# Optimization experiments

Hardware: AMD Instinct MI355X
Metric: run time of the kernel (lower is better)

## Reference

```python
import jax, jax.numpy as jnp
import numpy as np

NH = 4       # num_heads
WS = 4       # window_size (in subdomains)
SHIFT = 2    # shift (in subdomains) on odd layers
SUB = 16     # physical subdomain size (y and x)
L = 4        # num_layers
EPS = 1e-5   # InstanceNorm2d eps


def _pw_mlp(x, W1, b1, W2, b2):
    # pointwise (1x1 conv) MLP over channel dim of [..., C, y, x]
    h = jnp.einsum('oc,...cyx->...oyx', W1, x) + b1[:, None, None]
    h = jax.nn.gelu(h, approximate=False)
    return jnp.einsum('oc,...cyx->...oyx', W2, h) + b2[:, None, None]


def _inorm(x):
    # InstanceNorm2d (affine=False): normalize each channel over spatial dims
    mu = jnp.mean(x, axis=(-2, -1), keepdims=True)
    var = jnp.var(x, axis=(-2, -1), keepdims=True)
    return (x - mu) * jax.lax.rsqrt(var + EPS)


def _grid_to_win(g, B, nwy, nwx):
    # g: [B, n_sub_y, n_sub_x, C, sh, sw] -> [B*nwy*nwx, WS*WS, C, sh, sw]
    C, sh, sw = g.shape[3:]
    g = g.reshape(B, nwy, WS, nwx, WS, C, sh, sw).transpose(0, 1, 3, 2, 4, 5, 6, 7)
    return g.reshape(B * nwy * nwx, WS * WS, C, sh, sw)


def _win_to_grid(d, B, nwy, nwx):
    # inverse of _grid_to_win
    C, sh, sw = d.shape[2:]
    g = d.reshape(B, nwy, nwx, WS, WS, C, sh, sw).transpose(0, 1, 3, 2, 4, 5, 6, 7)
    return g.reshape(B, nwy * WS, nwx * WS, C, sh, sw)


def _attn(d, Wq, bq, Wk, bk, Wv, bv, Wo, bo, shift, B, nwy, nwx):
    # function-space windowed self-attention; tokens are subdomain functions
    if shift > 0:
        g = _win_to_grid(d, B, nwy, nwx)
        g = jnp.roll(g, (-shift, -shift), axis=(1, 2))
        d = _grid_to_win(g, B, nwy, nwx)
    E = Wq.shape[0]
    dh = E // NH
    Bw, S, C, sh, sw = d.shape

    def proj(W, b):
        p = jnp.einsum('dc,bscyx->bsdyx', W, d) + b[:, None, None]
        return p.reshape(Bw, S, NH, dh, sh, sw)

    q, k, vv = proj(Wq, bq), proj(Wk, bk), proj(Wv, bv)
    # integral inner-product score: mean over subdomain points, / sqrt(dh)
    scale = 1.0 / ((sh * sw) * (float(dh) ** 0.5))
    scores = jnp.einsum('bihcyx,bjhcyx->bhij', q, k) * scale
    A = jax.nn.softmax(scores, axis=-1)
    o = jnp.einsum('bhij,bjhcyx->bihcyx', A, vv).reshape(Bw, S, E, sh, sw)
    o = jnp.einsum('dc,bscyx->bsdyx', Wo, o) + bo[:, None, None]
    if shift > 0:
        g = _win_to_grid(o, B, nwy, nwx)
        g = jnp.roll(g, (shift, shift), axis=(1, 2))
        o = _grid_to_win(g, B, nwy, nwx)
    return o


def _forward(v, inp_W1, inp_b1, inp_W2, inp_b2, Wq, bq, Wk, bk, Wv, bv, Wo, bo,
             mlp_W1, mlp_b1, mlp_W2, mlp_b2, out_W1, out_b1, out_W2, out_b2,
             dsy, dsx):
    B, Cin, H, W = v.shape
    n_sub_y, n_sub_x = dsy // SUB, dsx // SUB
    sh, sw = H // n_sub_y, W // n_sub_x
    nwy, nwx = n_sub_y // WS, n_sub_x // WS
    # cell-centered grid, channels (y, x)
    yc = (jnp.arange(H, dtype=v.dtype) + 0.5) * (dsy / H)
    xc = (jnp.arange(W, dtype=v.dtype) + 0.5) * (dsx / W)
    g = jnp.stack(jnp.meshgrid(yc, xc, indexing='ij'), axis=0)  # [2,H,W]
    g = jnp.broadcast_to(g, (B, 2, H, W))
    v = jnp.concatenate([g, v], axis=1)
    v = _pw_mlp(v, inp_W1, inp_b1, inp_W2, inp_b2)  # [B,E,H,W]
    E = v.shape[1]
    # win_decompose2d: pixels -> subdomain grid -> windows of WSxWS subdomains
    sgrid = v.reshape(B, E, n_sub_y, sh, n_sub_x, sw).transpose(0, 2, 4, 1, 3, 5)
    d = _grid_to_win(sgrid, B, nwy, nwx)  # [B*nw, WS*WS, E, sh, sw]
    for i in range(L):
        shift = 0 if i % 2 == 0 else SHIFT
        d = _attn(_inorm(d), Wq[i], bq[i], Wk[i], bk[i], Wv[i], bv[i],
                  Wo[i], bo[i], shift, B, nwy, nwx) + d
        d = _pw_mlp(_inorm(d), mlp_W1[i], mlp_b1[i], mlp_W2[i], mlp_b2[i]) + d
    # win_recompose2d
    sgrid = _win_to_grid(d, B, nwy, nwx)  # [B, n_sub_y, n_sub_x, E, sh, sw]
    u = sgrid.transpose(0, 3, 1, 4, 2, 5).reshape(B, E, H, W)
    return _pw_mlp(u, out_W1, out_b1, out_W2, out_b2)


def setup_inputs() -> dict:
    key = jax.random.key(0)
    ks = jax.random.split(key, 16)
    B, Cin, H, W, E, HID, Cout = 8, 3, 256, 256, 64, 128, 1
    s = 0.02
    r = lambda k, shape: (s * jax.random.normal(k, shape)).astype(jnp.float32)
    z = lambda shape: jnp.zeros(shape, jnp.float32)
    return {
        'v': jax.random.normal(ks[0], (B, Cin, H, W), dtype=jnp.float32),
        'inp_W1': r(ks[1], (HID, Cin + 2)), 'inp_b1': z((HID,)),
        'inp_W2': r(ks[2], (E, HID)), 'inp_b2': z((E,)),
        'Wq': r(ks[3], (L, E, E)), 'bq': z((L, E)),
        'Wk': r(ks[4], (L, E, E)), 'bk': z((L, E)),
        'Wv': r(ks[5], (L, E, E)), 'bv': z((L, E)),
        'Wo': r(ks[6], (L, E, E)), 'bo': z((L, E)),
        'mlp_W1': r(ks[7], (L, E, E)), 'mlp_b1': z((L, E)),
        'mlp_W2': r(ks[8], (L, E, E)), 'mlp_b2': z((L, E)),
        'out_W1': r(ks[9], (HID, E)), 'out_b1': z((HID,)),
        'out_W2': r(ks[10], (Cout, HID)), 'out_b2': z((Cout,)),
        'domain_size_y': 256, 'domain_size_x': 256,
    }


def reference(v, inp_W1, inp_b1, inp_W2, inp_b2, Wq, bq, Wk, bk, Wv, bv, Wo, bo,
              mlp_W1, mlp_b1, mlp_W2, mlp_b2, out_W1, out_b1, out_W2, out_b2,
              domain_size_y, domain_size_x):
    return _forward(v, inp_W1, inp_b1, inp_W2, inp_b2, Wq, bq, Wk, bk, Wv, bv,
                    Wo, bo, mlp_W1, mlp_b1, mlp_W2, mlp_b2, out_W1, out_b1,
                    out_W2, out_b2, domain_size_y, domain_size_x)
```

## Files before the change

kernel.cpp:

```cpp
#include <hip/hip_runtime.h>
#include <math.h>

typedef unsigned short u16;
typedef unsigned int   u32;
typedef __attribute__((ext_vector_type(8))) short bf16x8;
typedef __attribute__((ext_vector_type(4))) float f32x4;

#define NTOK  2048
#define TOKSZ 16384ull

#define CBAR() __asm__ __volatile__("" ::: "memory")

__device__ __forceinline__ float bf2f(u16 b) { return __uint_as_float(((u32)b) << 16); }
__device__ __forceinline__ u16 f2bf(float f) {
    u32 u = __float_as_uint(f);
    u += 0x7FFFu + ((u >> 16) & 1u);
    return (u16)(u >> 16);
}
__device__ __forceinline__ float gelu_f(float x) {
    return 0.5f * x * (1.0f + erff(x * 0.70710678118654752440f));
}
__device__ __forceinline__ int shift_tok(int n) {
    int w = n >> 4, s = n & 15;
    int b = w >> 4, wy = (w >> 2) & 3, wx = w & 3;
// ... 78 lines not shown
            float ha = b1[hid] + W1[hid*5]*in0 + W1[hid*5+1]*in1 + W1[hid*5+2]*in2
                     + W1[hid*5+3]*in3 + W1[hid*5+4]*in4;
            float hb2 = b1[hid+1] + W1[hid*5+5]*in0 + W1[hid*5+6]*in1 + W1[hid*5+7]*in2
                     + W1[hid*5+8]*in3 + W1[hid*5+9]*in4;
            u32 pk = (u32)f2bf(gelu_f(ha)) | ((u32)f2bf(gelu_f(hb2)) << 16);
            *(u32*)&hsT[swz(t, h2 >> 3) + (h2 & 7)] = pk;
        }
        #pragma unroll
        for (int r = 0; r < 2; ++r) {
            int u = t + r * 256; int e = u >> 3, c8 = u & 7;
            *(uint4*)&wl[swz(e, c8)] = *(const uint4*)(W2bf + e * 128 + half * 64 + c8 * 8);
        }
        __syncthreads();
        #pragma unroll
        for (int ks = 0; ks < 2; ++ks) {
            U8 af[4], bf[4];
            #pragma unroll
            for (int mt = 0; mt < 4; ++mt)
                af[mt].u = *(const uint4*)&hsT[swz(px0 + mt*16 + m, ks*4 + qd)];
            #pragma unroll
            for (int nt = 0; nt < 4; ++nt)
                bf[nt].u = *(const uint4*)&wl[swz(nt*16 + m, ks*4 + qd)];
            #pragma unroll
            for (int mt = 0; mt < 4; ++mt)
                #pragma unroll
                for (int nt = 0; nt < 4; ++nt)
                    acc[mt][nt] = __builtin_amdgcn_mfma_f32_16x16x32_bf16(
                        af[mt].b, bf[nt].b, acc[mt][nt], 0, 0, 0);
        }
    }
    __syncthreads();
    float sv[4], qv[4];
    #pragma unroll
    for (int nt = 0; nt < 4; ++nt) {
        float ss = 0.f, qq = 0.f;
        #pragma unroll
        for (int mt = 0; mt < 4; ++mt)
            #pragma unroll
            for (int r = 0; r < 4; ++r) { float xx = acc[mt][nt][r]; ss += xx; qq = fmaf(xx, xx, qq); }
        ss += __shfl_xor(ss, 16); ss += __shfl_xor(ss, 32);
        qq += __shfl_xor(qq, 16); qq += __shfl_xor(qq, 32);
        sv[nt] = ss; qv[nt] = qq;
    }
    float* sarr = (float*)smem;
    if (qd == 0) {
        #pragma unroll
        for (int nt = 0; nt < 4; ++nt) {
            sarr[(nt*16 + m)*4 + wv] = sv[nt];
            sarr[256 + (nt*16 + m)*4 + wv] = qv[nt];
        }
    }
    __syncthreads();
    if (t < 64) {
        float ss = sarr[t*4] + sarr[t*4+1] + sarr[t*4+2] + sarr[t*4+3];
        float qq = sarr[256+t*4] + sarr[256+t*4+1] + sarr[256+t*4+2] + sarr[256+t*4+3];
        float mu = ss * (1.0f/256.0f);
        float var = qq * (1.0f/256.0f) - mu * mu;
        mursg[(size_t)n * 128 + t] = mu;
        mursg[(size_t)n * 128 + 64 + t] = rsqrtf(var + 1e-5f);
    }
    __syncthreads();
    float* eps = (float*)smem + wv * 2304;
    float* dp = d + (size_t)n * TOKSZ;
    #pragma unroll
    for (int ch2 = 0; ch2 < 2; ++ch2) {
        if (ch2) CBAR();
        #pragma unroll
        for (int mt = ch2*2; mt < ch2*2+2; ++mt)
            #pragma unroll
            for (int nt = 0; nt < 4; ++nt)
                #pragma unroll
                for (int r = 0; r < 4; ++r)
                    eps[((mt&1)*16 + qd*4 + r) * 68 + nt*16 + m] = acc[mt][nt][r];
        CBAR();
        #pragma unroll
        for (int j = 0; j < 8; ++j) {
            int f = l + 64*j; int row = f >> 4, c4 = f & 15;
            float4 v = *(float4*)&eps[row * 68 + c4 * 4];
            *(float4*)&dp[(px0 + ch2*32 + row) * 64 + c4 * 4] = v;
        }
    }
}

__device__ __forceinline__ void gemm64h(const u16* xs, const u16* wl, const float* bv4,
                                        int px0w, int m, int qd, u16* dst) {
    f32x4 acc[2][4];
    #pragma unroll
    for (int nt = 0; nt < 4; ++nt) {
        float bb = bv4[nt];
        acc[0][nt] = {bb, bb, bb, bb};
        acc[1][nt] = {bb, bb, bb, bb};
    }
    #pragma unroll
    for (int ks = 0; ks < 2; ++ks) {
        U8 af[2], bfr[4];
        #pragma unroll
        for (int mi = 0; mi < 2; ++mi)
            af[mi].u = *(const uint4*)&xs[swz(px0w + mi*16 + m, ks*4 + qd)];
        #pragma unroll
        for (int nt = 0; nt < 4; ++nt)
            bfr[nt].u = *(const uint4*)&wl[swz(nt*16 + m, ks*4 + qd)];
        #pragma unroll
        for (int mi = 0; mi < 2; ++mi)
            #pragma unroll
            for (int nt = 0; nt < 4; ++nt)
                acc[mi][nt] = __builtin_amdgcn_mfma_f32_16x16x32_bf16(
                    af[mi].b, bfr[nt].b, acc[mi][nt], 0, 0, 0);
    }
    #pragma unroll
    for (int mi = 0; mi < 2; ++mi)
        #pragma unroll
        for (int nt = 0; nt < 4; ++nt)
            #pragma unroll
            for (int r = 0; r < 4; ++r) {
                int R = px0w + mi*16 + qd*4 + r, ch = nt*16 + m;
                dst[swz(R, ch >> 3) + (ch & 7)] = f2bf(acc[mi][nt][r]);
            }
}

__global__ __launch_bounds__(256, 2)
void scores_qkv(const float* __restrict__ dres, const float* __restrict__ mursg,
                const u16* __restrict__ Wq, const float* __restrict__ bq,
                const u16* __restrict__ Wk, const float* __restrict__ bk,
                const u16* __restrict__ Wv, const float* __restrict__ bv,
                int shifted, float* __restrict__ Ap, u16* __restrict__ vbuf) {
    extern __shared__ char smem[];
    u16* xs  = (u16*)smem;
    u16* qls = (u16*)(smem + 16384);
    u16* kls = (u16*)(smem + 32768);
    u16* wlq = (u16*)(smem + 49152);
    u16* wlk = (u16*)(smem + 57344);
    u16* wlv = (u16*)(smem + 65536);
    float* mloc = (float*)(smem + 73728);
    int w = blockIdx.x, half = blockIdx.y, t = threadIdx.x;
    int wv = t >> 6, l = t & 63, m = l & 15, qd = l >> 4;
    int px0w = wv * 32;
    int nst[4];
    #pragma unroll
    for (int i8 = 0; i8 < 4; ++i8) {
        int nn = w * 16 + (4 * i8 + wv);
        nst[i8] = shifted ? shift_tok(nn) : nn;
    }
    #pragma unroll
    for (int r = 0; r < 8; ++r) {
        int u = t + r * 256;
        int nn = w * 16 + (u >> 7);
        int ni = shifted ? shift_tok(nn) : nn;
        mloc[u] = mursg[(size_t)ni * 128 + (u & 127)];
    }
    #pragma unroll
    for (int r = 0; r < 2; ++r) {
        int u = t + r * 256; int e = u >> 3, c8 = u & 7;
        *(uint4*)&wlq[swz(e, c8)] = *(const uint4*)(Wq + e * 64 + c8 * 8);
        *(uint4*)&wlk[swz(e, c8)] = *(const uint4*)(Wk + e * 64 + c8 * 8);
        *(uint4*)&wlv[swz(e, c8)] = *(const uint4*)(Wv + e * 64 + c8 * 8);
    }
    float bqv[4], bkv[4], bvv[4];
    #pragma unroll
    for (int nt = 0; nt < 4; ++nt) {
        bqv[nt] = bq[nt*16 + m]; bkv[nt] = bk[nt*16 + m]; bvv[nt] = bv[nt*16 + m];
    }
    f32x4 sacc = {0.f, 0.f, 0.f, 0.f};
    __syncthreads();
    for (int ch = 0; ch < 16; ++ch) {
        int pxb = half * 128 + ch * 8;
        #pragma unroll
        for (int i8 = 0; i8 < 4; ++i8) {
            int u = t + i8 * 256; int row = u >> 3, c8 = u & 7;
            int pxl = row & 7;
            int tok = 4 * i8 + wv;
            const float4* gp = (const float4*)
                (dres + (size_t)nst[i8] * TOKSZ + (size_t)(pxb + pxl) * 64 + c8 * 8);
            float4 f0 = gp[0], f1 = gp[1];
            const float4* mp = (const float4*)&mloc[tok * 128 + c8 * 8];
            float4 mu0 = mp[0], mu1 = mp[1];
            const float4* rp = (const float4*)&mloc[tok * 128 + 64 + c8 * 8];
            float4 rs0 = rp[0], rs1 = rp[1];
            uint4 o;
            o.x = (u32)f2bf((f0.x-mu0.x)*rs0.x) | ((u32)f2bf((f0.y-mu0.y)*rs0.y) << 16);
            o.y = (u32)f2bf((f0.z-mu0.z)*rs0.z) | ((u32)f2bf((f0.w-mu0.w)*rs0.w) << 16);
            o.z = (u32)f2bf((f1.x-mu1.x)*rs1.x) | ((u32)f2bf((f1.y-mu1.y)*rs1.y) << 16);
            o.w = (u32)f2bf((f1.z-mu1.z)*rs1.z) | ((u32)f2bf((f1.w-mu1.w)*rs1.w) << 16);
            *(uint4*)&xs[swz(row, c8)] = o;
        }
        __syncthreads();
        gemm64h(xs, wlq, bqv, px0w, m, qd, qls);
        gemm64h(xs, wlk, bkv, px0w, m, qd, kls);
        gemm64h(xs, wlv, bvv, px0w, m, qd, xs);
        __syncthreads();
        #pragma unroll
        for (int p2 = 0; p2 < 4; ++p2) {
            U8 af, bfr;
            int row = m * 8 + p2 * 2 + (qd >> 1);
            int c8 = wv * 2 + (qd & 1);
            af.u  = *(const uint4*)&qls[swz(row, c8)];
            bfr.u = *(const uint4*)&kls[swz(row, c8)];
            sacc = __builtin_amdgcn_mfma_f32_16x16x32_bf16(af.b, bfr.b, sacc, 0, 0, 0);
        }
        #pragma unroll
        for (int i8 = 0; i8 < 4; ++i8) {
            int u = t + i8 * 256; int row = u >> 3, c8 = u & 7;
            int pxl = row & 7;
            *(uint4*)(vbuf + (size_t)nst[i8] * 16384 + (size_t)(pxb + pxl) * 64 + c8 * 8)
                = *(const uint4*)&xs[swz(row, c8)];
        }
        __syncthreads();
    }
    float* ap = Ap + (size_t)half * 131072 + ((size_t)w * 4 + wv) * 256;
    #pragma unroll
    for (int r = 0; r < 4; ++r)
        ap[(qd * 4 + r) * 16 + m] = sacc[r] * (1.0f / 1024.0f);
}

__global__ __launch_bounds__(256, 2)
void wo_mlp(const u16* __restrict__ vb, const float* __restrict__ Ap,
            const u16* __restrict__ Wo, const float* __restrict__ bo,
            const u16* __restrict__ W1, const float* __restrict__ b1,
            const u16* __restrict__ W2, const float* __restrict__ b2,
            int shifted, float* __restrict__ dres, float* __restrict__ mursg,
            int wmu) {
    extern __shared__ char smem[];
    u16* xs = (u16*)smem;
    u16* wl = (u16*)(smem + 32768);
    float* As = (float*)(smem + 32768);
    int*  nis = (int*)(smem + 33792);
    float* sarr = (float*)(smem + 32768);
    float* murs2 = (float*)smem;
    int bid = blockIdx.x;
    int qg = bid >> 7, r7 = bid & 127;
    int n = ((qg << 3) + (r7 & 7)) * 16 + (r7 >> 3);
    int t = threadIdx.x;
    int wv = t >> 6, l = t & 63, m = l & 15, qd = l >> 4;
    int px0 = wv * 64;
    int w = n >> 4, i = n & 15;
    int no = shifted ? shift_tok(n) : n;
    int rbase = l >> 4, c4l = l & 15;
    if (t < 16) { int nn = w * 16 + t; nis[t] = shifted ? shift_tok(nn) : nn; }
    if (t >= 64 && t < 128) {
        int u = t - 64; int h = u >> 4, j = u & 15;
        size_t ai = ((size_t)(w * 4 + h)) * 256 + i * 16 + j;
        float sc = (Ap[ai] + Ap[131072 + ai]) * (1.0f / 1024.0f);
        float mx = sc;
        #pragma unroll
        for (int off = 1; off < 16; off <<= 1) mx = fmaxf(mx, __shfl_xor(mx, off, 16));
        float e = expf(sc - mx);
        float ssum = e;
        #pragma unroll
        for (int off = 1; off < 16; off <<= 1) ssum += __shfl_xor(ssum, off, 16);
        As[u] = e / ssum;
    }
    __syncthreads();
    #pragma unroll
    for (int r = 0; r < 8; ++r) {
        int idx = r * 256 + t;
        int px = idx >> 3, c8 = idx & 7, h = c8 >> 1;
        float a0=0,a1=0,a2=0,a3=0,a4=0,a5=0,a6=0,a7=0;
        #pragma unroll
        for (int j = 0; j < 16; ++j) {
            const u16* src = vb + (size_t)nis[j] * 16384 + (size_t)px * 64 + c8 * 8;
            uint4 pv = *(const uint4*)src;
            float aw = As[h * 16 + j];
            a0 = fmaf(aw, __uint_as_float(pv.x << 16), a0);
            a1 = fmaf(aw, __uint_as_float(pv.x & 0xFFFF0000u), a1);
            a2 = fmaf(aw, __uint_as_float(pv.y << 16), a2);
            a3 = fmaf(aw, __uint_as_float(pv.y & 0xFFFF0000u), a3);
            a4 = fmaf(aw, __uint_as_float(pv.z << 16), a4);
            a5 = fmaf(aw, __uint_as_float(pv.z & 0xFFFF0000u), a5);
            a6 = fmaf(aw, __uint_as_float(pv.w << 16), a6);
            a7 = fmaf(aw, __uint_as_float(pv.w & 0xFFFF0000u), a7);
        }
        uint4 o;
        o.x = (u32)f2bf(a0) | ((u32)f2bf(a1) << 16);
        o.y = (u32)f2bf(a2) | ((u32)f2bf(a3) << 16);
        o.z = (u32)f2bf(a4) | ((u32)f2bf(a5) << 16);
        o.w = (u32)f2bf(a6) | ((u32)f2bf(a7) << 16);
        *(uint4*)&xs[swz(px, c8)] = o;
    }
    __syncthreads();
    #pragma unroll
    for (int r = 0; r < 2; ++r) {
        int u = t + r * 256;
        int e = u >> 3, c8 = u & 7;
        *(uint4*)&wl[swz(e, c8)] = *(const uint4*)(Wo + e * 64 + c8 * 8);
    }
    __syncthreads();
    f32x4 acc[4][4];
    #pragma unroll
    for (int nt = 0; nt < 4; ++nt) {
        float bb = bo[nt * 16 + m];
        #pragma unroll
        for (int mt = 0; mt < 4; ++mt) acc[mt][nt] = {bb, bb, bb, bb};
    }
    #pragma unroll
    for (int ks = 0; ks < 2; ++ks) {
// ... 115 lines not shown
                int R = px0 + mt*16 + qd*4 + r;
                xs[swz(R, ch >> 3) + (ch & 7)] = f2bf(gelu_f(acc[mt][nt][r]));
            }
    }
    #pragma unroll
    for (int r = 0; r < 2; ++r) {
        int u = t + r * 256;
        int e = u >> 3, c8 = u & 7;
        *(uint4*)&wl[swz(e, c8)] = *(const uint4*)(W2 + e * 64 + c8 * 8);
    }
    __syncthreads();
    #pragma unroll
    for (int nt = 0; nt < 4; ++nt) {
        float bb = b2[nt * 16 + m];
        #pragma unroll
        for (int mt = 0; mt < 4; ++mt) acc[mt][nt] = {bb, bb, bb, bb};
    }
    #pragma unroll
    for (int ks = 0; ks < 2; ++ks) {
        U8 af[4], bf[4];
        #pragma unroll
        for (int mt = 0; mt < 4; ++mt)
            af[mt].u = *(const uint4*)&xs[swz(px0 + mt*16 + m, ks*4 + qd)];
        #pragma unroll
        for (int nt = 0; nt < 4; ++nt)
            bf[nt].u = *(const uint4*)&wl[swz(nt*16 + m, ks*4 + qd)];
        #pragma unroll
        for (int mt = 0; mt < 4; ++mt)
            #pragma unroll
            for (int nt = 0; nt < 4; ++nt)
                acc[mt][nt] = __builtin_amdgcn_mfma_f32_16x16x32_bf16(
                    af[mt].b, bf[nt].b, acc[mt][nt], 0, 0, 0);
    }
    __syncthreads();
    #pragma unroll
    for (int ch2 = 0; ch2 < 2; ++ch2) {
        if (ch2) CBAR();
        #pragma unroll
        for (int mt = ch2*2; mt < ch2*2+2; ++mt)
            #pragma unroll
            for (int nt = 0; nt < 4; ++nt)
                #pragma unroll
                for (int r = 0; r < 4; ++r)
                    eps[((mt&1)*16 + qd*4 + r) * 68 + nt*16 + m] = acc[mt][nt][r];
        CBAR();
        #pragma unroll
        for (int j = 0; j < 8; ++j) {
            int row = rbase + 4*j;
            float4 dv = *(float4*)&eps[row * 68 + c4l * 4];
            float4 bs = xv[ch2][j];
            bs.x += dv.x; bs.y += dv.y; bs.z += dv.z; bs.w += dv.w;
            xv[ch2][j] = bs;
            *(float4*)&dp[(px0 + ch2*32 + row) * 64 + c4l * 4] = bs;
        }
    }
    if (wmu) {
        __syncthreads();
        float t0=0,t1=0,t2=0,t3=0,u0=0,u1=0,u2=0,u3=0;
        #pragma unroll
        for (int ch2 = 0; ch2 < 2; ++ch2)
            #pragma unroll
            for (int j = 0; j < 8; ++j) {
                float4 v = xv[ch2][j];
                t0 += v.x; u0 = fmaf(v.x, v.x, u0);
                t1 += v.y; u1 = fmaf(v.y, v.y, u1);
                t2 += v.z; u2 = fmaf(v.z, v.z, u2);
                t3 += v.w; u3 = fmaf(v.w, v.w, u3);
            }
        sarr[(cb+0)*16+g]=t0; sarr[(cb+1)*16+g]=t1; sarr[(cb+2)*16+g]=t2; sarr[(cb+3)*16+g]=t3;
        qarr[(cb+0)*16+g]=u0; qarr[(cb+1)*16+g]=u1; qarr[(cb+2)*16+g]=u2; qarr[(cb+3)*16+g]=u3;
        __syncthreads();
        if (t < 64) {
            float ss = 0.f, qq = 0.f;
            #pragma unroll
            for (int gg = 0; gg < 16; ++gg) { ss += sarr[t*16+gg]; qq += qarr[t*16+gg]; }
            float mu = ss * (1.0f/256.0f);
            float var = qq * (1.0f/256.0f) - mu * mu;
            mursg[(size_t)no * 128 + t] = mu;
            mursg[(size_t)no * 128 + 64 + t] = rsqrtf(var + 1e-5f);
        }
    }
}

__global__ __launch_bounds__(256, 3)
void wo_av(const u16* __restrict__ vb, const float* __restrict__ Ap,
           const u16* __restrict__ Wo, const float* __restrict__ bo,
           int shifted, float* __restrict__ dres) {
    extern __shared__ char smem[];
    u16* xs = (u16*)smem;
    u16* wl = (u16*)(smem + 32768);
    float* As = (float*)(smem + 40960);
    int*  nis = (int*)(smem + 41216);
    int bid = blockIdx.x;
    int qg = bid >> 7, r7 = bid & 127;
    int n = ((qg << 3) + (r7 & 7)) * 16 + (r7 >> 3);
    int t = threadIdx.x;
    int wv = t >> 6, l = t & 63, m = l & 15, qd = l >> 4;
    int px0 = wv * 64;
    int w = n >> 4, i = n & 15;
    int no = shifted ? shift_tok(n) : n;
    if (t < 16) { int nn = w * 16 + t; nis[t] = shifted ? shift_tok(nn) : nn; }
    if (t >= 64 && t < 128) {
        int u = t - 64; int h = u >> 4, j = u & 15;
        size_t ai = ((size_t)(w * 4 + h)) * 256 + i * 16 + j;
        float sc = (Ap[ai] + Ap[131072 + ai]) * (1.0f / 1024.0f);
        float mx = sc;
        #pragma unroll
        for (int off = 1; off < 16; off <<= 1) mx = fmaxf(mx, __shfl_xor(mx, off, 16));
        float e = expf(sc - mx);
        float ssum = e;
        #pragma unroll
        for (int off = 1; off < 16; off <<= 1) ssum += __shfl_xor(ssum, off, 16);
        As[u] = e / ssum;
    }
    #pragma unroll
    for (int r = 0; r < 2; ++r) {
        int u = t + r * 256;
        int e = u >> 3, c8 = u & 7;
        *(uint4*)&wl[swz(e, c8)] = *(const uint4*)(Wo + e * 64 + c8 * 8);
    }
    __syncthreads();
    #pragma unroll
    for (int r = 0; r < 8; ++r) {
        int idx = r * 256 + t;
        int px = idx >> 3, c8 = idx & 7, h = c8 >> 1;
        float a0=0,a1=0,a2=0,a3=0,a4=0,a5=0,a6=0,a7=0;
        #pragma unroll
        for (int j = 0; j < 16; ++j) {
            const u16* src = vb + (size_t)nis[j] * 16384 + (size_t)px * 64 + c8 * 8;
            uint4 pv = *(const uint4*)src;
            float aw = As[h * 16 + j];
            a0 = fmaf(aw, __uint_as_float(pv.x << 16), a0);
            a1 = fmaf(aw, __uint_as_float(pv.x & 0xFFFF0000u), a1);
            a2 = fmaf(aw, __uint_as_float(pv.y << 16), a2);
            a3 = fmaf(aw, __uint_as_float(pv.y & 0xFFFF0000u), a3);
            a4 = fmaf(aw, __uint_as_float(pv.z << 16), a4);
            a5 = fmaf(aw, __uint_as_float(pv.z & 0xFFFF0000u), a5);
            a6 = fmaf(aw, __uint_as_float(pv.w << 16), a6);
            a7 = fmaf(aw, __uint_as_float(pv.w & 0xFFFF0000u), a7);
        }
        uint4 o;
        o.x = (u32)f2bf(a0) | ((u32)f2bf(a1) << 16);
        o.y = (u32)f2bf(a2) | ((u32)f2bf(a3) << 16);
        o.z = (u32)f2bf(a4) | ((u32)f2bf(a5) << 16);
        o.w = (u32)f2bf(a6) | ((u32)f2bf(a7) << 16);
        *(uint4*)&xs[swz(px, c8)] = o;
    }
    __syncthreads();
    f32x4 acc[4][4];
    #pragma unroll
    for (int nt = 0; nt < 4; ++nt) {
        float bb = bo[nt * 16 + m];
        #pragma unroll
        for (int mt = 0; mt < 4; ++mt) acc[mt][nt] = {bb, bb, bb, bb};
    }
    #pragma unroll
    for (int ks = 0; ks < 2; ++ks) {
        U8 af[4], bf[4];
        #pragma unroll
        for (int mt = 0; mt < 4; ++mt)
            af[mt].u = *(const uint4*)&xs[swz(px0 + mt*16 + m, ks*4 + qd)];
        #pragma unroll
        for (int nt = 0; nt < 4; ++nt)
            bf[nt].u = *(const uint4*)&wl[swz(nt*16 + m, ks*4 + qd)];
        #pragma unroll
        for (int mt = 0; mt < 4; ++mt)
            #pragma unroll
            for (int nt = 0; nt < 4; ++nt)
                acc[mt][nt] = __builtin_amdgcn_mfma_f32_16x16x32_bf16(
                    af[mt].b, bf[nt].b, acc[mt][nt], 0, 0, 0);
    }
    __syncthreads();
    float* eps = (float*)smem + wv * 2304;
    float* dp = dres + (size_t)no * TOKSZ;
    #pragma unroll
    for (int ch2 = 0; ch2 < 2; ++ch2) {
        if (ch2) CBAR();
        #pragma unroll
        for (int mt = ch2*2; mt < ch2*2+2; ++mt)
            #pragma unroll
            for (int nt = 0; nt < 4; ++nt)
                #pragma unroll
                for (int r = 0; r < 4; ++r)
                    eps[((mt&1)*16 + qd*4 + r) * 68 + nt*16 + m] = acc[mt][nt][r];
        CBAR();
        #pragma unroll
        for (int j = 0; j < 8; ++j) {
            int f = l + 64*j; int row = f >> 4, c4 = f & 15;
            float4 dv = *(float4*)&eps[row * 68 + c4 * 4];
            float* gp = &dp[(px0 + ch2*32 + row) * 64 + c4 * 4];
            float4 gv = *(float4*)gp;
            gv.x += dv.x; gv.y += dv.y; gv.z += dv.z; gv.w += dv.w;
            *(float4*)gp = gv;
        }
    }
}

__global__ __launch_bounds__(256, 2)
void mlp_out(const float* __restrict__ dres,
             const u16* __restrict__ W1, const float* __restrict__ b1,
             const u16* __restrict__ W2, const float* __restrict__ b2,
             const u16* __restrict__ oW1, const float* __restrict__ ob1,
             const float* __restrict__ oW2, const float* __restrict__ ob2,
             void* __restrict__ outp, const int* __restrict__ flag) {
    extern __shared__ char smem[];
    u16* xs = (u16*)smem;
    u16* wl = (u16*)(smem + 32768);
    float* sarr = (float*)(smem + 32768);
    float* murs = (float*)smem;
    int n = blockIdx.x, t = threadIdx.x;
    int wv = t >> 6, l = t & 63, m = l & 15, qd = l >> 4;
    int px0 = wv * 64;
    int rbase = l >> 4, c4 = l & 15;
    const float4* gin = (const float4*)(dres + (size_t)n * TOKSZ);
    float4 xv[2][8];
    float s0=0,s1=0,s2=0,s3=0,q0=0,q1=0,q2=0,q3=0;
    #pragma unroll
    for (int ch2 = 0; ch2 < 2; ++ch2)
        #pragma unroll
        for (int j = 0; j < 8; ++j) {
            float4 v = gin[(px0 + ch2*32 + rbase + 4*j) * 16 + c4];
            xv[ch2][j] = v;
            s0 += v.x; q0 = fmaf(v.x, v.x, q0);
            s1 += v.y; q1 = fmaf(v.y, v.y, q1);
            s2 += v.z; q2 = fmaf(v.z, v.z, q2);
            s3 += v.w; q3 = fmaf(v.w, v.w, q3);
        }
    int cb = 4 * c4, g = t >> 4;
    sarr[(cb+0)*16+g]=s0; sarr[(cb+1)*16+g]=s1; sarr[(cb+2)*16+g]=s2; sarr[(cb+3)*16+g]=s3;
    float* qarr = sarr + 1024;
    qarr[(cb+0)*16+g]=q0; qarr[(cb+1)*16+g]=q1; qarr[(cb+2)*16+g]=q2; qarr[(cb+3)*16+g]=q3;
    __syncthreads();
    if (t < 64) {
        float ss = 0.f, qq = 0.f;
        #pragma unroll
        for (int gg = 0; gg < 16; ++gg) { ss += sarr[t*16+gg]; qq += qarr[t*16+gg]; }
        float mu = ss * (1.0f/256.0f);
        float var = qq * (1.0f/256.0f) - mu * mu;
        murs[t] = mu; murs[64 + t] = rsqrtf(var + 1e-5f);
    }
    __syncthreads();
    float m0 = murs[cb], m1 = murs[cb+1], m2 = murs[cb+2], m3 = murs[cb+3];
    float r0 = murs[64+cb], r1 = murs[64+cb+1], r2 = murs[64+cb+2], r3 = murs[64+cb+3];
    __syncthreads();
    #pragma unroll
    for (int ch2 = 0; ch2 < 2; ++ch2)
        #pragma unroll
        for (int j = 0; j < 8; ++j) {
            float4 v = xv[ch2][j];
            int row = px0 + ch2*32 + rbase + 4*j;
            uint2 o;
            o.x = (u32)f2bf((v.x-m0)*r0) | ((u32)f2bf((v.y-m1)*r1) << 16);
            o.y = (u32)f2bf((v.z-m2)*r2) | ((u32)f2bf((v.w-m3)*r3) << 16);
            *(uint2*)&xs[swz(row, c4 >> 1) + (c4 & 1) * 4] = o;
        }
    #pragma unroll
    for (int r = 0; r < 2; ++r) {
        int u = t + r * 256;
        int e = u >> 3, c8 = u & 7;
        *(uint4*)&wl[swz(e, c8)] = *(const uint4*)(W1 + e * 64 + c8 * 8);
    }
    __syncthreads();
    f32x4 acc[4][4];
    #pragma unroll
    for (int nt = 0; nt < 4; ++nt) {
        float bb = b1[nt * 16 + m];
        #pragma unroll
        for (int mt = 0; mt < 4; ++mt) acc[mt][nt] = {bb, bb, bb, bb};
    }
    #pragma unroll
    for (int ks = 0; ks < 2; ++ks) {
        U8 af[4], bf[4];
        #pragma unroll
        for (int mt = 0; mt < 4; ++mt)
            af[mt].u = *(const uint4*)&xs[swz(px0 + mt*16 + m, ks*4 + qd)];
        #pragma unroll
        for (int nt = 0; nt < 4; ++nt)
            bf[nt].u = *(const uint4*)&wl[swz(nt*16 + m, ks*4 + qd)];
        #pragma unroll
        for (int mt = 0; mt < 4; ++mt)
            #pragma unroll
            for (int nt = 0; nt < 4; ++nt)
                acc[mt][nt] = __builtin_amdgcn_mfma_f32_16x16x32_bf16(
                    af[mt].b, bf[nt].b, acc[mt][nt], 0, 0, 0);
    }
    __syncthreads();
    #pragma unroll
    for (int nt = 0; nt < 4; ++nt) {
        int ch = nt * 16 + m;
        #pragma unroll
        for (int mt = 0; mt < 4; ++mt)
            #pragma unroll
            for (int r = 0; r < 4; ++r) {
                int R = px0 + mt*16 + qd*4 + r;
                xs[swz(R, ch >> 3) + (ch & 7)] = f2bf(gelu_f(acc[mt][nt][r]));
            }
    }
    #pragma unroll
    for (int r = 0; r < 2; ++r) {
        int u = t + r * 256;
        int e = u >> 3, c8 = u & 7;
        *(uint4*)&wl[swz(e, c8)] = *(const uint4*)(W2 + e * 64 + c8 * 8);
    }
    __syncthreads();
    #pragma unroll
    for (int nt = 0; nt < 4; ++nt) {
        float bb = b2[nt * 16 + m];
        #pragma unroll
        for (int mt = 0; mt < 4; ++mt) acc[mt][nt] = {bb, bb, bb, bb};
    }
    #pragma unroll
    for (int ks = 0; ks < 2; ++ks) {
        U8 af[4], bf[4];
        #pragma unroll
        for (int mt = 0; mt < 4; ++mt)
            af[mt].u = *(const uint4*)&xs[swz(px0 + mt*16 + m, ks*4 + qd)];
        #pragma unroll
        for (int nt = 0; nt < 4; ++nt)
            bf[nt].u = *(const uint4*)&wl[swz(nt*16 + m, ks*4 + qd)];
        #pragma unroll
        for (int mt = 0; mt < 4; ++mt)
            #pragma unroll
            for (int nt = 0; nt < 4; ++nt)
                acc[mt][nt] = __builtin_amdgcn_mfma_f32_16x16x32_bf16(
                    af[mt].b, bf[nt].b, acc[mt][nt], 0, 0, 0);
    }
    __syncthreads();
    float* eps = (float*)smem + wv * 2304;
    #pragma unroll
    for (int ch2 = 0; ch2 < 2; ++ch2) {
        if (ch2) CBAR();
        #pragma unroll
        for (int mt = ch2*2; mt < ch2*2+2; ++mt)
            #pragma unroll
            for (int nt = 0; nt < 4; ++nt)
                #pragma unroll
                for (int r = 0; r < 4; ++r)
                    eps[((mt&1)*16 + qd*4 + r) * 68 + nt*16 + m] = acc[mt][nt][r];
        CBAR();
        #pragma unroll
        for (int j = 0; j < 8; ++j) {
            int row = rbase + 4*j;
            float4 dv = *(float4*)&eps[row * 68 + c4 * 4];
            float4 bs = xv[ch2][j];
            bs.x += dv.x; bs.y += dv.y; bs.z += dv.z; bs.w += dv.w;
            xv[ch2][j] = bs;
        }
    }
    __syncthreads();
    #pragma unroll
    for (int ch2 = 0; ch2 < 2; ++ch2)
        #pragma unroll
        for (int j = 0; j < 8; ++j) {
            float4 v = xv[ch2][j];
            int row = px0 + ch2*32 + rbase + 4*j;
            uint2 o;
            o.x = (u32)f2bf(v.x) | ((u32)f2bf(v.y) << 16);
            o.y = (u32)f2bf(v.z) | ((u32)f2bf(v.w) << 16);
            *(uint2*)&xs[swz(row, c4 >> 1) + (c4 & 1) * 4] = o;
        }
    __syncthreads();
    float val[4][4];
    #pragma unroll
    for (int mt = 0; mt < 4; ++mt)
        #pragma unroll
        for (int r = 0; r < 4; ++r) val[mt][r] = 0.f;
    for (int nh = 0; nh < 2; ++nh) {
        if (nh) __syncthreads();
        #pragma unroll
        for (int r = 0; r < 2; ++r) {
            int u = t + r * 256;
            int e = u >> 3, c8 = u & 7;
            *(uint4*)&wl[swz(e, c8)] = *(const uint4*)(oW1 + (size_t)nh * 4096 + e * 64 + c8 * 8);
        }
        __syncthreads();
        float w2v[4];
        #pragma unroll
        for (int nt = 0; nt < 4; ++nt) w2v[nt] = oW2[nh * 64 + nt * 16 + m];
        #pragma unroll
        for (int mtp = 0; mtp < 2; ++mtp) {
            f32x4 oacc[2][4];
            #pragma unroll
            for (int nt = 0; nt < 4; ++nt) {
                float bb = ob1[nh * 64 + nt * 16 + m];
                oacc[0][nt] = {bb, bb, bb, bb};
                oacc[1][nt] = {bb, bb, bb, bb};
            }
            #pragma unroll
            for (int ks = 0; ks < 2; ++ks) {
                U8 af[2], bf[4];
                #pragma unroll
                for (int mi = 0; mi < 2; ++mi)
                    af[mi].u = *(const uint4*)&xs[swz(px0 + (2*mtp+mi)*16 + m, ks*4 + qd)];
                #pragma unroll
                for (int nt = 0; nt < 4; ++nt)
                    bf[nt].u = *(const uint4*)&wl[swz(nt*16 + m, ks*4 + qd)];
                #pragma unroll
                for (int mi = 0; mi < 2; ++mi)
                    #pragma unroll
                    for (int nt = 0; nt < 4; ++nt)
                        oacc[mi][nt] = __builtin_amdgcn_mfma_f32_16x16x32_bf16(
                            af[mi].b, bf[nt].b, oacc[mi][nt], 0, 0, 0);
            }
            #pragma unroll
            for (int mi = 0; mi < 2; ++mi)
                #pragma unroll
                for (int r = 0; r < 4; ++r) {
                    float p = 0.f;
                    #pragma unroll
                    for (int nt = 0; nt < 4; ++nt)
                        p = fmaf(gelu_f(oacc[mi][nt][r]), w2v[nt], p);
                    val[2*mtp + mi][r] += p;
                }
        }
    }
    __syncthreads();
    float* red = (float*)smem;
    #pragma unroll
    for (int mt = 0; mt < 4; ++mt)
        #pragma unroll
        for (int r = 0; r < 4; ++r)
            red[(px0 + mt*16 + qd*4 + r) * 17 + m] = val[mt][r];
    __syncthreads();
    float a = ob2[0];
    #pragma unroll
    for (int j = 0; j < 16; ++j) a += red[t * 17 + j];
    int w = n >> 4, s = n & 15;
    int b = w >> 4, wy = (w >> 2) & 3, wx = w & 3;
    int ty = s >> 2, tx = s & 3;
    int y = ((wy << 2) + ty) * 16 + (t >> 4);
    int x = ((wx << 2) + tx) * 16 + (t & 15);
    size_t oi = (size_t)b * 65536 + (size_t)y * 256 + (size_t)x;
    if (*flag) ((float*)outp)[oi] = a;
    else       ((u16*)outp)[oi] = f2bf(a);
}

extern "C" void kernel_launch(void* const* d_in, const int* in_sizes, int n_in,
                              void* d_out, int out_size, void* d_ws, size_t ws_size,
                              hipStream_t stream) {
    (void)n_in; (void)out_size; (void)ws_size;
    const int* pdsy = (const int*)d_in[21];
    const int* pdsx = (const int*)d_in[22];

    char* wsb = (char*)d_ws;
    float* bufd  = (float*)wsb;
    u16*  vbuf   = (u16*)(wsb + 134217728ull);
    float* Ap    = (float*)(wsb + 201326592ull);
    float* mursg = (float*)(wsb + 202375168ull);
    float* wbufA = (float*)(wsb + 203423744ull);
    u16* wbuf16  = (u16*)(wsb + 203434496ull);
    int* flag    = (int*)(wsb + 203669248ull);

    const int f32set[12] = {1, 2, 4, 6, 8, 10, 12, 14, 16, 18, 19, 20};
    WArgs wa;
    int off16[NWT + 1]; off16[0] = 0;
    int c32[NWT + 1];
    int fo = 0;
    for (int i = 0; i < NWT; ++i) {
        int di = i + 1;
        wa.src[i] = d_in[di];
        off16[i + 1] = off16[i] + in_sizes[di];
        wa.off16[i] = off16[i];
        int isf = 0;
        for (int j = 0; j < 12; ++j) if (f32set[j] == di) isf = 1;
        wa.f32o[i] = isf ? fo : -1;
        c32[di] = isf ? fo : -1;
        if (isf) fo += in_sizes[di];
    }
    wa.off16[NWT] = off16[NWT];

    detect_kernel<<<1, 64, 0, stream>>>((const u16*)d_in[1], flag);
    cvt_weights<<<(off16[NWT] + 255) / 256, 256, 0, stream>>>(wa, flag, wbufA, wbuf16);

    const float* f_inpW1 = wbufA + c32[1];
    const float* f_inpb1 = wbufA + c32[2];
    const float* f_inpb2 = wbufA + c32[4];
    const float* f_bq  = wbufA + c32[6];
    const float* f_bk  = wbufA + c32[8];
    const float* f_bv  = wbufA + c32[10];
    const float* f_bo  = wbufA + c32[12];
    const float* f_mb1 = wbufA + c32[14];
    const float* f_mb2 = wbufA + c32[16];
    const float* f_ob1 = wbufA + c32[18];
    const float* f_oW2 = wbufA + c32[19];
    const float* f_ob2 = wbufA + c32[20];
    const u16* h_inpW2 = wbuf16 + off16[2];
    const u16* h_Wq  = wbuf16 + off16[4];
    const u16* h_Wk  = wbuf16 + off16[6];
    const u16* h_Wv  = wbuf16 + off16[8];
    const u16* h_Wo  = wbuf16 + off16[10];
    const u16* h_mW1 = wbuf16 + off16[12];
    const u16* h_mW2 = wbuf16 + off16[14];
    const u16* h_oW1 = wbuf16 + off16[16];

    embed_mfma<<<NTOK, 256, 40960, stream>>>(d_in[0], flag, f_inpW1, f_inpb1,
                                             h_inpW2, f_inpb2, pdsy, pdsx,
                                             bufd, mursg);

    for (int l = 0; l < 4; ++l) {
        int sh = l & 1;
        const u16* Wql = h_Wq + l * 4096;  const float* bql = f_bq + l * 64;
        const u16* Wkl = h_Wk + l * 4096;  const float* bkl = f_bk + l * 64;
        const u16* Wvl = h_Wv + l * 4096;  const float* bvl = f_bv + l * 64;
        const u16* Wol = h_Wo + l * 4096;  const float* bol = f_bo + l * 64;
        const u16* W1l = h_mW1 + l * 4096; const float* b1l = f_mb1 + l * 64;
        const u16* W2l = h_mW2 + l * 4096; const float* b2l = f_mb2 + l * 64;

        scores_qkv<<<dim3(128, 2), 256, 81920, stream>>>(
            bufd, mursg, Wql, bql, Wkl, bkl, Wvl, bvl, sh, Ap, vbuf);
        if (l < 3) {
            wo_mlp<<<NTOK, 256, 40960, stream>>>(vbuf, Ap, Wol, bol,
                                                 W1l, b1l, W2l, b2l,
                                                 sh, bufd, mursg, 1);
        } else {
            wo_av<<<NTOK, 256, 41280, stream>>>(vbuf, Ap, Wol, bol, sh, bufd);
            mlp_out<<<NTOK, 256, 40960, stream>>>(bufd, W1l, b1l, W2l, b2l,
                                                  h_oW1, f_ob1, f_oW2, f_ob2,
                                                  d_out, flag);
        }
    }
}
```

Measured before the change: 957.6 us.

## Double threads per block in scores_qkv and split score reduction across waves

scores_qkv now launches 512 threads (8 waves) instead of 256, so each wave computes a 16-row tile of the QKV projections instead of 32 rows. The per-head score MFMAs are split across two wave groups, and their partial sums are combined through shared memory at the end. The aim is more latency hiding and parallelism per block on the 256-block grid, which is small relative to the CU count. The cost is an extra barrier plus shared-memory traffic for the reduction, and higher register pressure under the tighter launch bounds.

```diff
diff --git a/kernel.cpp b/kernel.cpp
--- a/kernel.cpp
+++ b/kernel.cpp
@@ -184,43 +184,36 @@
     }
 }
 
-__device__ __forceinline__ void gemm64h(const u16* xs, const u16* wl, const float* bv4,
+__device__ __forceinline__ void gemm64q(const u16* xs, const u16* wl, const float* bv4,
                                         int px0w, int m, int qd, u16* dst) {
-    f32x4 acc[2][4];
+    f32x4 acc[4];
     #pragma unroll
     for (int nt = 0; nt < 4; ++nt) {
         float bb = bv4[nt];
-        acc[0][nt] = {bb, bb, bb, bb};
-        acc[1][nt] = {bb, bb, bb, bb};
+        acc[nt] = {bb, bb, bb, bb};
     }
     #pragma unroll
     for (int ks = 0; ks < 2; ++ks) {
-        U8 af[2], bfr[4];
-        #pragma unroll
-        for (int mi = 0; mi < 2; ++mi)
-            af[mi].u = *(const uint4*)&xs[swz(px0w + mi*16 + m, ks*4 + qd)];
+        U8 af, bfr[4];
+        af.u = *(const uint4*)&xs[swz(px0w + m, ks*4 + qd)];
         #pragma unroll
         for (int nt = 0; nt < 4; ++nt)
             bfr[nt].u = *(const uint4*)&wl[swz(nt*16 + m, ks*4 + qd)];
         #pragma unroll
-        for (int mi = 0; mi < 2; ++mi)
-            #pragma unroll
-            for (int nt = 0; nt < 4; ++nt)
-                acc[mi][nt] = __builtin_amdgcn_mfma_f32_16x16x32_bf16(
-                    af[mi].b, bfr[nt].b, acc[mi][nt], 0, 0, 0);
-    }
-    #pragma unroll
-    for (int mi = 0; mi < 2; ++mi)
-        #pragma unroll
         for (int nt = 0; nt < 4; ++nt)
-            #pragma unroll
-            for (int r = 0; r < 4; ++r) {
-                int R = px0w + mi*16 + qd*4 + r, ch = nt*16 + m;
-                dst[swz(R, ch >> 3) + (ch & 7)] = f2bf(acc[mi][nt][r]);
-            }
-}
-
-__global__ __launch_bounds__(256, 2)
+            acc[nt] = __builtin_amdgcn_mfma_f32_16x16x32_bf16(
+                af.b, bfr[nt].b, acc[nt], 0, 0, 0);
+    }
+    #pragma unroll
+    for (int nt = 0; nt < 4; ++nt)
+        #pragma unroll
+        for (int r = 0; r < 4; ++r) {
+            int R = px0w + qd*4 + r, ch = nt*16 + m;
+            dst[swz(R, ch >> 3) + (ch & 7)] = f2bf(acc[nt][r]);
+        }
+}
+
+__global__ __launch_bounds__(512, 4)
 void scores_qkv(const float* __restrict__ dres, const float* __restrict__ mursg,
                 const u16* __restrict__ Wq, const float* __restrict__ bq,
                 const u16* __restrict__ Wk, const float* __restrict__ bk,
@@ -236,23 +229,23 @@
     float* mloc = (float*)(smem + 73728);
     int w = blockIdx.x, half = blockIdx.y, t = threadIdx.x;
     int wv = t >> 6, l = t & 63, m = l & 15, qd = l >> 4;
-    int px0w = wv * 32;
-    int nst[4];
-    #pragma unroll
-    for (int i8 = 0; i8 < 4; ++i8) {
-        int nn = w * 16 + (4 * i8 + wv);
+    int px0w = wv * 16;
+    int h = wv & 3, pp = wv >> 2;
+    int nst[2];
+    #pragma unroll
+    for (int i8 = 0; i8 < 2; ++i8) {
+        int nn = w * 16 + (wv + 8 * i8);
         nst[i8] = shifted ? shift_tok(nn) : nn;
     }
     #pragma unroll
-    for (int r = 0; r < 8; ++r) {
-        int u = t + r * 256;
+    for (int r = 0; r < 4; ++r) {
+        int u = t + r * 512;
         int nn = w * 16 + (u >> 7);
         int ni = shifted ? shift_tok(nn) : nn;
         mloc[u] = mursg[(size_t)ni * 128 + (u & 127)];
     }
-    #pragma unroll
-    for (int r = 0; r < 2; ++r) {
-        int u = t + r * 256; int e = u >> 3, c8 = u & 7;
+    {
+        int e = t >> 3, c8 = t & 7;
         *(uint4*)&wlq[swz(e, c8)] = *(const uint4*)(Wq + e * 64 + c8 * 8);
         *(uint4*)&wlk[swz(e, c8)] = *(const uint4*)(Wk + e * 64 + c8 * 8);
         *(uint4*)&wlv[swz(e, c8)] = *(const uint4*)(Wv + e * 64 + c8 * 8);
@@ -267,10 +260,10 @@
     for (int ch = 0; ch < 16; ++ch) {
         int pxb = half * 128 + ch * 8;
         #pragma unroll
-        for (int i8 = 0; i8 < 4; ++i8) {
-            int u = t + i8 * 256; int row = u >> 3, c8 = u & 7;
+        for (int i8 = 0; i8 < 2; ++i8) {
+            int u = t + i8 * 512; int row = u >> 3, c8 = u & 7;
             int pxl = row & 7;
-            int tok = 4 * i8 + wv;
+            int tok = wv + 8 * i8;
             const float4* gp = (const float4*)
                 (dres + (size_t)nst[i8] * TOKSZ + (size_t)(pxb + pxl) * 64 + c8 * 8);
             float4 f0 = gp[0], f1 = gp[1];
@@ -286,32 +279,43 @@
             *(uint4*)&xs[swz(row, c8)] = o;
         }
         __syncthreads();
-        gemm64h(xs, wlq, bqv, px0w, m, qd, qls);
-        gemm64h(xs, wlk, bkv, px0w, m, qd, kls);
-        gemm64h(xs, wlv, bvv, px0w, m, qd, xs);
+        gemm64q(xs, wlq, bqv, px0w, m, qd, qls);
+        gemm64q(xs, wlk, bkv, px0w, m, qd, kls);
+        gemm64q(xs, wlv, bvv, px0w, m, qd, xs);
         __syncthreads();
         #pragma unroll
-        for (int p2 = 0; p2 < 4; ++p2) {
+        for (int p2i = 0; p2i < 2; ++p2i) {
+            int p2 = pp * 2 + p2i;
             U8 af, bfr;
             int row = m * 8 + p2 * 2 + (qd >> 1);
-            int c8 = wv * 2 + (qd & 1);
+            int c8 = h * 2 + (qd & 1);
             af.u  = *(const uint4*)&qls[swz(row, c8)];
             bfr.u = *(const uint4*)&kls[swz(row, c8)];
             sacc = __builtin_amdgcn_mfma_f32_16x16x32_bf16(af.b, bfr.b, sacc, 0, 0, 0);
         }
         #pragma unroll
-        for (int i8 = 0; i8 < 4; ++i8) {
-            int u = t + i8 * 256; int row = u >> 3, c8 = u & 7;
+        for (int i8 = 0; i8 < 2; ++i8) {
+            int u = t + i8 * 512; int row = u >> 3, c8 = u & 7;
             int pxl = row & 7;
             *(uint4*)(vbuf + (size_t)nst[i8] * 16384 + (size_t)(pxb + pxl) * 64 + c8 * 8)
                 = *(const uint4*)&xs[swz(row, c8)];
         }
         __syncthreads();
     }
-    float* ap = Ap + (size_t)half * 131072 + ((size_t)w * 4 + wv) * 256;
-    #pragma unroll
-    for (int r = 0; r < 4; ++r)
-        ap[(qd * 4 + r) * 16 + m] = sacc[r] * (1.0f / 1024.0f);
+    float* pc = (float*)qls;
+    if (pp) {
+        #pragma unroll
+        for (int r = 0; r < 4; ++r) pc[(h * 64 + l) * 4 + r] = sacc[r];
+    }
+    __syncthreads();
+    if (!pp) {
+        float* ap = Ap + (size_t)half * 131072 + ((size_t)w * 4 + h) * 256;
+        #pragma unroll
+        for (int r = 0; r < 4; ++r) {
+            float sv = sacc[r] + pc[(h * 64 + l) * 4 + r];
+            ap[(qd * 4 + r) * 16 + m] = sv * (1.0f / 1024.0f);
+        }
+    }
 }
 
 __global__ __launch_bounds__(256, 2)
@@ -1017,7 +1021,7 @@
         const u16* W1l = h_mW1 + l * 4096; const float* b1l = f_mb1 + l * 64;
         const u16* W2l = h_mW2 + l * 4096; const float* b2l = f_mb2 + l * 64;
 
-        scores_qkv<<<dim3(128, 2), 256, 81920, stream>>>(
+        scores_qkv<<<dim3(128, 2), 512, 81920, stream>>>(
             bufd, mursg, Wql, bql, Wkl, bkl, Wvl, bvl, sh, Ap, vbuf);
         if (l < 3) {
             wo_mlp<<<NTOK, 256, 40960, stream>>>(vbuf, Ap, Wol, bol,
```

Measured after the change: 989.6 us. +3.3%, slower.

## Fuse final-layer Wo attention output with MLP and output head kernel

Applied to the files above, without the earlier changes.

Merges the last layer's wo_av and mlp_out kernels into one kernel. The residual sum stays in registers instead of being written back to the global buffer and read again. The output pixel index now uses the unshifted token mapping, and shared memory is remapped so the Wo weights load after the AV stage, which adds one extra barrier. Occupancy hint drops from 3 to 2 blocks per CU for this stage.

```diff
diff --git a/kernel.cpp b/kernel.cpp
--- a/kernel.cpp
+++ b/kernel.cpp
@@ -593,15 +593,22 @@
     }
 }
 
-__global__ __launch_bounds__(256, 3)
-void wo_av(const u16* __restrict__ vb, const float* __restrict__ Ap,
-           const u16* __restrict__ Wo, const float* __restrict__ bo,
-           int shifted, float* __restrict__ dres) {
+__global__ __launch_bounds__(256, 2)
+void wo_mlp_out(const u16* __restrict__ vb, const float* __restrict__ Ap,
+                const u16* __restrict__ Wo, const float* __restrict__ bo,
+                const u16* __restrict__ W1, const float* __restrict__ b1,
+                const u16* __restrict__ W2, const float* __restrict__ b2,
+                int shifted, const float* __restrict__ dres,
+                const u16* __restrict__ oW1, const float* __restrict__ ob1,
+                const float* __restrict__ oW2, const float* __restrict__ ob2,
+                void* __restrict__ outp, const int* __restrict__ flag) {
     extern __shared__ char smem[];
     u16* xs = (u16*)smem;
     u16* wl = (u16*)(smem + 32768);
-    float* As = (float*)(smem + 40960);
-    int*  nis = (int*)(smem + 41216);
+    float* As = (float*)(smem + 32768);
+    int*  nis = (int*)(smem + 33792);
+    float* sarr = (float*)(smem + 32768);
+    float* murs2 = (float*)smem;
     int bid = blockIdx.x;
     int qg = bid >> 7, r7 = bid & 127;
     int n = ((qg << 3) + (r7 & 7)) * 16 + (r7 >> 3);
@@ -610,6 +617,7 @@
     int px0 = wv * 64;
     int w = n >> 4, i = n & 15;
     int no = shifted ? shift_tok(n) : n;
+    int rbase = l >> 4, c4l = l & 15;
     if (t < 16) { int nn = w * 16 + t; nis[t] = shifted ? shift_tok(nn) : nn; }
     if (t >= 64 && t < 128) {
         int u = t - 64; int h = u >> 4, j = u & 15;
@@ -623,12 +631,6 @@
         #pragma unroll
         for (int off = 1; off < 16; off <<= 1) ssum += __shfl_xor(ssum, off, 16);
         As[u] = e / ssum;
-    }
-    #pragma unroll
-    for (int r = 0; r < 2; ++r) {
-        int u = t + r * 256;
-        int e = u >> 3, c8 = u & 7;
-        *(uint4*)&wl[swz(e, c8)] = *(const uint4*)(Wo + e * 64 + c8 * 8);
     }
     __syncthreads();
     #pragma unroll
@@ -658,6 +660,13 @@
         *(uint4*)&xs[swz(px, c8)] = o;
     }
     __syncthreads();
+    #pragma unroll
+    for (int r = 0; r < 2; ++r) {
+        int u = t + r * 256;
+        int e = u >> 3, c8 = u & 7;
+        *(uint4*)&wl[swz(e, c8)] = *(const uint4*)(Wo + e * 64 + c8 * 8);
+    }
+    __syncthreads();
     f32x4 acc[4][4];
     #pragma unroll
     for (int nt = 0; nt < 4; ++nt) {
@@ -683,7 +692,8 @@
     }
     __syncthreads();
     float* eps = (float*)smem + wv * 2304;
-    float* dp = dres + (size_t)no * TOKSZ;
+    const float* dp = dres + (size_t)no * TOKSZ;
+    float4 xv[2][8];
     #pragma unroll
     for (int ch2 = 0; ch2 < 2; ++ch2) {
         if (ch2) CBAR();
@@ -697,49 +707,28 @@
         CBAR();
         #pragma unroll
         for (int j = 0; j < 8; ++j) {
-            int f = l + 64*j; int row = f >> 4, c4 = f & 15;
-            float4 dv = *(float4*)&eps[row * 68 + c4 * 4];
-            float* gp = &dp[(px0 + ch2*32 + row) * 64 + c4 * 4];
-            float4 gv = *(float4*)gp;
+            int row = rbase + 4*j;
+            float4 dv = *(float4*)&eps[row * 68 + c4l * 4];
+            float4 gv = *(const float4*)&dp[(px0 + ch2*32 + row) * 64 + c4l * 4];
             gv.x += dv.x; gv.y += dv.y; gv.z += dv.z; gv.w += dv.w;
-            *(float4*)gp = gv;
-        }
-    }
-}
-
-__global__ __launch_bounds__(256, 2)
-void mlp_out(const float* __restrict__ dres,
-             const u16* __restrict__ W1, const float* __restrict__ b1,
-             const u16* __restrict__ W2, const float* __restrict__ b2,
-             const u16* __restrict__ oW1, const float* __restrict__ ob1,
-             const float* __restrict__ oW2, const float* __restrict__ ob2,
-             void* __restrict__ outp, const int* __restrict__ flag) {
-    extern __shared__ char smem[];
-    u16* xs = (u16*)smem;
-    u16* wl = (u16*)(smem + 32768);
-    float* sarr = (float*)(smem + 32768);
-    float* murs = (float*)smem;
-    int n = blockIdx.x, t = threadIdx.x;
-    int wv = t >> 6, l = t & 63, m = l & 15, qd = l >> 4;
-    int px0 = wv * 64;
-    int rbase = l >> 4, c4 = l & 15;
-    const float4* gin = (const float4*)(dres + (size_t)n * TOKSZ);
-    float4 xv[2][8];
+            xv[ch2][j] = gv;
+        }
+    }
+    __syncthreads();
     float s0=0,s1=0,s2=0,s3=0,q0=0,q1=0,q2=0,q3=0;
     #pragma unroll
     for (int ch2 = 0; ch2 < 2; ++ch2)
         #pragma unroll
         for (int j = 0; j < 8; ++j) {
-            float4 v = gin[(px0 + ch2*32 + rbase + 4*j) * 16 + c4];
-            xv[ch2][j] = v;
+            float4 v = xv[ch2][j];
             s0 += v.x; q0 = fmaf(v.x, v.x, q0);
             s1 += v.y; q1 = fmaf(v.y, v.y, q1);
             s2 += v.z; q2 = fmaf(v.z, v.z, q2);
             s3 += v.w; q3 = fmaf(v.w, v.w, q3);
         }
-    int cb = 4 * c4, g = t >> 4;
+    int cb = 4 * c4l, g = t >> 4;
+    float* qarr = sarr + 1024;
     sarr[(cb+0)*16+g]=s0; sarr[(cb+1)*16+g]=s1; sarr[(cb+2)*16+g]=s2; sarr[(cb+3)*16+g]=s3;
-    float* qarr = sarr + 1024;
     qarr[(cb+0)*16+g]=q0; qarr[(cb+1)*16+g]=q1; qarr[(cb+2)*16+g]=q2; qarr[(cb+3)*16+g]=q3;
     __syncthreads();
     if (t < 64) {
@@ -748,11 +737,11 @@
         for (int gg = 0; gg < 16; ++gg) { ss += sarr[t*16+gg]; qq += qarr[t*16+gg]; }
         float mu = ss * (1.0f/256.0f);
         float var = qq * (1.0f/256.0f) - mu * mu;
-        murs[t] = mu; murs[64 + t] = rsqrtf(var + 1e-5f);
-    }
-    __syncthreads();
-    float m0 = murs[cb], m1 = murs[cb+1], m2 = murs[cb+2], m3 = murs[cb+3];
-    float r0 = murs[64+cb], r1 = murs[64+cb+1], r2 = murs[64+cb+2], r3 = murs[64+cb+3];
+        murs2[t] = mu; murs2[64 + t] = rsqrtf(var + 1e-5f);
+    }
+    __syncthreads();
+    float m0 = murs2[cb], m1 = murs2[cb+1], m2 = murs2[cb+2], m3 = murs2[cb+3];
+    float r0 = murs2[64+cb], r1 = murs2[64+cb+1], r2 = murs2[64+cb+2], r3 = murs2[64+cb+3];
     __syncthreads();
     #pragma unroll
     for (int ch2 = 0; ch2 < 2; ++ch2)
@@ -763,7 +752,7 @@
             uint2 o;
             o.x = (u32)f2bf((v.x-m0)*r0) | ((u32)f2bf((v.y-m1)*r1) << 16);
             o.y = (u32)f2bf((v.z-m2)*r2) | ((u32)f2bf((v.w-m3)*r3) << 16);
-            *(uint2*)&xs[swz(row, c4 >> 1) + (c4 & 1) * 4] = o;
+            *(uint2*)&xs[swz(row, c4l >> 1) + (c4l & 1) * 4] = o;
         }
     #pragma unroll
     for (int r = 0; r < 2; ++r) {
@@ -772,7 +761,6 @@
         *(uint4*)&wl[swz(e, c8)] = *(const uint4*)(W1 + e * 64 + c8 * 8);
     }
     __syncthreads();
-    f32x4 acc[4][4];
     #pragma unroll
     for (int nt = 0; nt < 4; ++nt) {
         float bb = b1[nt * 16 + m];
@@ -837,7 +825,6 @@
                     af[mt].b, bf[nt].b, acc[mt][nt], 0, 0, 0);
     }
     __syncthreads();
-    float* eps = (float*)smem + wv * 2304;
     #pragma unroll
     for (int ch2 = 0; ch2 < 2; ++ch2) {
         if (ch2) CBAR();
@@ -852,7 +839,7 @@
         #pragma unroll
         for (int j = 0; j < 8; ++j) {
             int row = rbase + 4*j;
-            float4 dv = *(float4*)&eps[row * 68 + c4 * 4];
+            float4 dv = *(float4*)&eps[row * 68 + c4l * 4];
             float4 bs = xv[ch2][j];
             bs.x += dv.x; bs.y += dv.y; bs.z += dv.z; bs.w += dv.w;
             xv[ch2][j] = bs;
@@ -868,7 +855,7 @@
             uint2 o;
             o.x = (u32)f2bf(v.x) | ((u32)f2bf(v.y) << 16);
             o.y = (u32)f2bf(v.z) | ((u32)f2bf(v.w) << 16);
-            *(uint2*)&xs[swz(row, c4 >> 1) + (c4 & 1) * 4] = o;
+            *(uint2*)&xs[swz(row, c4l >> 1) + (c4l & 1) * 4] = o;
         }
     __syncthreads();
     float val[4][4];
@@ -936,9 +923,9 @@
     float a = ob2[0];
     #pragma unroll
     for (int j = 0; j < 16; ++j) a += red[t * 17 + j];
-    int w = n >> 4, s = n & 15;
-    int b = w >> 4, wy = (w >> 2) & 3, wx = w & 3;
-    int ty = s >> 2, tx = s & 3;
+    int wp = no >> 4, sp = no & 15;
+    int b = wp >> 4, wy = (wp >> 2) & 3, wx = wp & 3;
+    int ty = sp >> 2, tx = sp & 3;
     int y = ((wy << 2) + ty) * 16 + (t >> 4);
     int x = ((wx << 2) + tx) * 16 + (t & 15);
     size_t oi = (size_t)b * 65536 + (size_t)y * 256 + (size_t)x;
@@ -1024,10 +1011,11 @@
                                                  W1l, b1l, W2l, b2l,
                                                  sh, bufd, mursg, 1);
         } else {
-            wo_av<<<NTOK, 256, 41280, stream>>>(vbuf, Ap, Wol, bol, sh, bufd);
-            mlp_out<<<NTOK, 256, 40960, stream>>>(bufd, W1l, b1l, W2l, b2l,
-                                                  h_oW1, f_ob1, f_oW2, f_ob2,
-                                                  d_out, flag);
-        }
-    }
-}
+            wo_mlp_out<<<NTOK, 256, 40960, stream>>>(vbuf, Ap, Wol, bol,
+                                                     W1l, b1l, W2l, b2l,
+                                                     sh, bufd,
+                                                     h_oW1, f_ob1, f_oW2, f_ob2,
+                                                     d_out, flag);
+        }
+    }
+}
```

After: 935.9 us. 1.02x faster.
